# Kernel optimization log

Hardware: AMD Instinct MI355X
Metric: run time of the kernel (lower is better)

The kernel has to match this reference:

```python
import jax, jax.numpy as jnp
import numpy as np

N = 20000      # nodes
E = 320000     # edges (before self loops)
DIN = 64       # input feature dim
C = 256        # hidden_dim (per-head channels)
HEADS = 4
NEG_SLOPE_ATT = 0.2   # GATv2 leaky_relu slope
NEG_SLOPE = 0.01      # torch F.leaky_relu default


def setup_inputs() -> dict:
    key = jax.random.key(0)
    ks = jax.random.split(key, 32)
    def g(i, shape, fan_in):
        return jax.random.normal(ks[i], shape, jnp.float32) * (1.0 / np.sqrt(fan_in))
    inp = {}
    inp["x"] = jax.random.normal(ks[0], (N, DIN), jnp.float32)
    inp["src"] = jax.random.randint(ks[1], (E,), 0, N, jnp.int32)
    inp["dst"] = jax.random.randint(ks[2], (E,), 0, N, jnp.int32)
    # input layer
    inp["W_in"] = g(3, (DIN, C), DIN); inp["b_in"] = jnp.zeros((C,), jnp.float32)
    # conv1: in=256 -> heads=4, out=256, concat
    inp["Wl1"] = g(4, (C, HEADS * C), C); inp["bl1"] = jnp.zeros((HEADS * C,), jnp.float32)
    inp["Wr1"] = g(5, (C, HEADS * C), C); inp["br1"] = jnp.zeros((HEADS * C,), jnp.float32)
    inp["att1"] = g(6, (HEADS, C), C); inp["bias1"] = jnp.zeros((HEADS * C,), jnp.float32)
    # conv2: in=1024 -> heads=4, out=256, concat
    inp["Wl2"] = g(7, (HEADS * C, HEADS * C), HEADS * C); inp["bl2"] = jnp.zeros((HEADS * C,), jnp.float32)
    inp["Wr2"] = g(8, (HEADS * C, HEADS * C), HEADS * C); inp["br2"] = jnp.zeros((HEADS * C,), jnp.float32)
    inp["att2"] = g(9, (HEADS, C), C); inp["bias2"] = jnp.zeros((HEADS * C,), jnp.float32)
    # conv3: in=1024 -> heads=1, out=256, no concat
    inp["Wl3"] = g(10, (HEADS * C, C), HEADS * C); inp["bl3"] = jnp.zeros((C,), jnp.float32)
    inp["Wr3"] = g(11, (HEADS * C, C), HEADS * C); inp["br3"] = jnp.zeros((C,), jnp.float32)
    inp["att3"] = g(12, (1, C), C); inp["bias3"] = jnp.zeros((C,), jnp.float32)
    # output layer
    inp["W_out"] = g(13, (C, 1), C); inp["b_out"] = jnp.zeros((1,), jnp.float32)
    return inp


def _seg_softmax(scores, seg, n):
    # scores: [E, H] segment-wise softmax over dst node ids
    m = jax.ops.segment_max(scores, seg, num_segments=n)
    ex = jnp.exp(scores - m[seg])
    den = jax.ops.segment_sum(ex, seg, num_segments=n)
    return ex / den[seg]


def _gatv2(x, s, d, Wl, bl, Wr, br, att, bias, heads, concat):
    n = x.shape[0]
    c = att.shape[1]
    xl = (x @ Wl + bl).reshape(n, heads, c)  # messages (source side)
    xr = (x @ Wr + br).reshape(n, heads, c)  # target side
    e = jax.nn.leaky_relu(xl[s] + xr[d], NEG_SLOPE_ATT)          # [E, H, C]
    sc = jnp.einsum('ehc,hc->eh', e, att)                         # [E, H]
    alpha = _seg_softmax(sc, d, n)                                # [E, H]
    out = jax.ops.segment_sum(alpha[:, :, None] * xl[s], d, num_segments=n)  # [N, H, C]
    out = out.reshape(n, heads * c) if concat else out.mean(axis=1)
    return out + bias


def reference(x, src, dst, W_in, b_in, Wl1, bl1, Wr1, br1, att1, bias1,
              Wl2, bl2, Wr2, br2, att2, bias2, Wl3, bl3, Wr3, br3, att3, bias3,
              W_out, b_out):
    n = x.shape[0]
    loop = jnp.arange(n, dtype=src.dtype)
    s = jnp.concatenate([src, loop])  # add_self_loops=True (PyG default)
    d = jnp.concatenate([dst, loop])
    h = jax.nn.leaky_relu(x @ W_in + b_in, NEG_SLOPE)
    h1 = jax.nn.elu(_gatv2(h, s, d, Wl1, bl1, Wr1, br1, att1, bias1, HEADS, True))
    h2 = jax.nn.elu(_gatv2(h1, s, d, Wl2, bl2, Wr2, br2, att2, bias2, HEADS, True))
    h3 = _gatv2(h2, s, d, Wl3, bl3, Wr3, br3, att3, bias3, 1, False)
    out = jax.nn.leaky_relu(h3, NEG_SLOPE) + h
    logits = (out @ W_out + b_out).squeeze(-1)
    return logits
```

## Files before the change

kernel.cpp:

```cpp
#include <hip/hip_runtime.h>
#include <math.h>

#define NEG_ATT 0.2f
#define NEG 0.01f

typedef __attribute__((ext_vector_type(8))) short short8;
typedef __attribute__((ext_vector_type(4))) float f32x4;

static __device__ __forceinline__ float lrelu(float x, float s) { return x > 0.f ? x : s * x; }
static __device__ __forceinline__ unsigned short f2b(float f) {
  union { float f; unsigned int i; } v; v.f = f;
  unsigned int r = (v.i + 0x7fffu + ((v.i >> 16) & 1u)) >> 16;
  return (unsigned short)r;
}
static __device__ __forceinline__ void unpack8(uint4 r, float* x) {
  union { unsigned int u; float f; } t;
  t.u = r.x << 16;          x[0] = t.f;
  t.u = r.x & 0xffff0000u;  x[1] = t.f;
  t.u = r.y << 16;          x[2] = t.f;
  t.u = r.y & 0xffff0000u;  x[3] = t.f;
  t.u = r.z << 16;          x[4] = t.f;
  t.u = r.z & 0xffff0000u;  x[5] = t.f;
  t.u = r.w << 16;          x[6] = t.f;
  t.u = r.w & 0xffff0000u;  x[7] = t.f;
}

__global__ void zero_int_kernel(int* __restrict__ p, int n) {
  int i = blockIdx.x * blockDim.x + threadIdx.x;
  if (i < n) p[i] = 0;
}

__global__ void hist_kernel(const int* __restrict__ dst, int* __restrict__ cnt, int E, int N) {
  int i = blockIdx.x * blockDim.x + threadIdx.x;
  int tot = E + N;
  if (i >= tot) return;
  int d = (i < E) ? dst[i] : (i - E);
  atomicAdd(&cnt[d], 1);
}

__global__ void scan_kernel(const int* __restrict__ cnt, int* __restrict__ rowptr,
                            int* __restrict__ cursor, int n) {
  __shared__ int wsum[16];
  __shared__ int carry_s;
  int t = threadIdx.x;
  int lane = t & 63, wv = t >> 6;
  if (t == 0) carry_s = 0;
  __syncthreads();
  for (int base = 0; base < n; base += 1024) {
    int i = base + t;
    int orig = (i < n) ? cnt[i] : 0;
    int v = orig;
    #pragma unroll
    for (int off = 1; off < 64; off <<= 1) {
      int u = __shfl_up(v, off);
      if (lane >= off) v += u;
    }
    if (lane == 63) wsum[wv] = v;
    __syncthreads();
    if (t < 16) {
      int s = wsum[t];
      #pragma unroll
      for (int off = 1; off < 16; off <<= 1) {
        int u = __shfl_up(s, off);
        if (t >= off) s += u;
      }
      wsum[t] = s;
    }
    __syncthreads();
    int waveoff = (wv > 0) ? wsum[wv - 1] : 0;
    int carry = carry_s;
    int excl = carry + waveoff + v - orig;
    if (i < n) { rowptr[i] = excl; cursor[i] = excl; }
    __syncthreads();
    if (t == 0) carry_s = carry + wsum[15];
    __syncthreads();
  }
  if (t == 0) rowptr[n] = carry_s;
}

__global__ void fill_kernel(const int* __restrict__ src, const int* __restrict__ dst,
                            int* __restrict__ cursor, int* __restrict__ colsrc, int E, int N) {
  int i = blockIdx.x * blockDim.x + threadIdx.x;
  int tot = E + N;
  if (i >= tot) return;
  int d, s;
  if (i < E) { d = dst[i]; s = src[i]; } else { d = i - E; s = i - E; }
  int pos = atomicAdd(&cursor[d], 1);
  colsrc[pos] = s;
}

static __device__ __forceinline__ void do_transpose(
    const float* __restrict__ W, unsigned short* __restrict__ Wt,
    int K, int Ncol, int lbid, float (*t)[33]) {
  int nxb = Ncol >> 5;
  int bx = lbid % nxb, by = lbid / nxb;
  int n0 = bx * 32, k0 = by * 32;
  int tx = threadIdx.x & 31, ty = threadIdx.x >> 5;
  #pragma unroll
  for (int i = 0; i < 4; ++i)
    t[ty + i * 8][tx] = W[(size_t)(k0 + ty + i * 8) * Ncol + n0 + tx];
  __syncthreads();
  #pragma unroll
  for (int i = 0; i < 4; ++i)
    Wt[(size_t)(n0 + ty + i * 8) * K + k0 + tx] = f2b(t[tx][ty + i * 8]);
}

__global__ __launch_bounds__(256) void prep_all(
    const float* __restrict__ W_in,
    const float* __restrict__ Wl1, const float* __restrict__ Wr1,
    const float* __restrict__ Wl2, const float* __restrict__ Wr2,
    const float* __restrict__ Wl3, const float* __restrict__ Wr3,
    unsigned short* __restrict__ WtIn,
    unsigned short* __restrict__ WtL1, unsigned short* __restrict__ WtR1,
    unsigned short* __restrict__ WtL2, unsigned short* __restrict__ WtR2,
    unsigned short* __restrict__ WtL3, unsigned short* __restrict__ WtR3,
    const float* __restrict__ x, unsigned short* __restrict__ xbf, int nx_elems,
    const float* __restrict__ bl1, const float* __restrict__ br1,
    const float* __restrict__ bl2, const float* __restrict__ br2,
    const float* __restrict__ bl3, const float* __restrict__ br3,
    float* __restrict__ bLR1, float* __restrict__ bLR2, float* __restrict__ bLR3) {
  __shared__ float t[32][33];
  int bid = blockIdx.x;
  if (bid < 16)        { do_transpose(W_in, WtIn, 64, 256, bid, t); return; }
  if (bid < 272)       { do_transpose(Wl1, WtL1, 256, 1024, bid - 16, t); return; }
  if (bid < 528)       { do_transpose(Wr1, WtR1, 256, 1024, bid - 272, t); return; }
  if (bid < 1552)      { do_transpose(Wl2, WtL2, 1024, 1024, bid - 528, t); return; }
  if (bid < 2576)      { do_transpose(Wr2, WtR2, 1024, 1024, bid - 1552, t); return; }
  if (bid < 2832)      { do_transpose(Wl3, WtL3, 1024, 256, bid - 2576, t); return; }
  if (bid < 3088)      { do_transpose(Wr3, WtR3, 1024, 256, bid - 2832, t); return; }
  if (bid < 3106) {
    int i = (bid - 3088) * 256 + threadIdx.x;
    if (i < 1024)      bLR1[i] = bl1[i];
    else if (i < 2048) bLR1[i] = br1[i - 1024];
    else if (i < 3072) bLR2[i - 2048] = bl2[i - 2048];
    else if (i < 4096) bLR2[i - 2048] = br2[i - 3072];
    else if (i < 4352) bLR3[i - 4096] = bl3[i - 4096];
    else if (i < 4608) bLR3[i - 4096] = br3[i - 4352];
    return;
  }
  int i = (bid - 3106) * 256 + threadIdx.x;
  if (i < nx_elems) xbf[i] = f2b(x[i]);
}

__global__ __launch_bounds__(256) void gemm_mfma(
    const unsigned short* __restrict__ A, const unsigned short* __restrict__ Bt,
    const float* __restrict__ bias, float* __restrict__ Cf, unsigned short* __restrict__ Cb,
    int M, int K, int ldcf, int ldcb, int act) {
  __shared__ __align__(16) unsigned short As[128 * 64];
  __shared__ __align__(16) unsigned short Bs[128 * 64];
  int tid = threadIdx.x;
  int wave = tid >> 6, lane = tid & 63;
  int wm = wave >> 1, wn = wave & 1;
  int quad = lane >> 4, l16 = lane & 15;
  int row0 = blockIdx.y * 128, col0 = blockIdx.x * 128;
  int r0 = tid >> 2, seg0 = tid & 3;
  int swz = (seg0 ^ ((r0 >> 1) & 3)) * 8;
  int wsl0 = r0 * 64 + swz;
  int wsl1 = wsl0 + 32;
  int wsl2 = wsl0 + 64 * 64;
  int wsl3 = wsl2 + 32;
  int chunkbase = (quad ^ ((l16 >> 1) & 3)) * 8;

  const unsigned short* gA = A + (size_t)(row0 + r0) * K + seg0 * 8;
  const unsigned short* gB = Bt + (size_t)(col0 + r0) * K + seg0 * 8;
  const size_t rstep = (size_t)64 * K;

  f32x4 acc[4][4];
  #pragma unroll
  for (int i = 0; i < 4; ++i)
    #pragma unroll
    for (int j = 0; j < 4; ++j)
      acc[i][j] = (f32x4){0.f, 0.f, 0.f, 0.f};

  uint4 pa0 = *(const uint4*)(gA);
  uint4 pa1 = *(const uint4*)(gA + 32);
  uint4 pa2 = *(const uint4*)(gA + rstep);
  uint4 pa3 = *(const uint4*)(gA + rstep + 32);
  uint4 pb0 = *(const uint4*)(gB);
  uint4 pb1 = *(const uint4*)(gB + 32);
  uint4 pb2 = *(const uint4*)(gB + rstep);
  uint4 pb3 = *(const uint4*)(gB + rstep + 32);

  for (int k0 = 0; k0 < K; k0 += 64) {
    *(uint4*)&As[wsl0] = pa0;
    *(uint4*)&As[wsl1] = pa1;
    *(uint4*)&As[wsl2] = pa2;
    *(uint4*)&As[wsl3] = pa3;
    *(uint4*)&Bs[wsl0] = pb0;
    *(uint4*)&Bs[wsl1] = pb1;
    *(uint4*)&Bs[wsl2] = pb2;
    *(uint4*)&Bs[wsl3] = pb3;
    __syncthreads();
    int kn = k0 + 64;
    if (kn < K) {
      pa0 = *(const uint4*)(gA + kn);
      pa1 = *(const uint4*)(gA + kn + 32);
      pa2 = *(const uint4*)(gA + kn + rstep);
      pa3 = *(const uint4*)(gA + kn + rstep + 32);
      pb0 = *(const uint4*)(gB + kn);
      pb1 = *(const uint4*)(gB + kn + 32);
      pb2 = *(const uint4*)(gB + kn + rstep);
      pb3 = *(const uint4*)(gB + kn + rstep + 32);
    }
    #pragma unroll
    for (int h = 0; h < 2; ++h) {
      short8 afr[4], bfr[4];
      #pragma unroll
      for (int t = 0; t < 4; ++t) {
        afr[t] = *(const short8*)&As[(wm * 64 + t * 16 + l16) * 64 + h * 32 + chunkbase];
        bfr[t] = *(const short8*)&Bs[(wn * 64 + t * 16 + l16) * 64 + h * 32 + chunkbase];
      }
      #pragma unroll
      for (int mt = 0; mt < 4; ++mt)
        #pragma unroll
        for (int nt = 0; nt < 4; ++nt)
          acc[mt][nt] = __builtin_amdgcn_mfma_f32_16x16x32_bf16(afr[mt], bfr[nt], acc[mt][nt], 0, 0, 0);
    }
    __syncthreads();
  }

  #pragma unroll
  for (int mt = 0; mt < 4; ++mt) {
    #pragma unroll
    for (int r = 0; r < 4; ++r) {
      int row = row0 + wm * 64 + mt * 16 + quad * 4 + r;
      if (row >= M) continue;
      #pragma unroll
      for (int nt = 0; nt < 4; ++nt) {
        int col = col0 + wn * 64 + nt * 16 + l16;
        float v = acc[mt][nt][r] + bias[col];
        if (act == 1) v = lrelu(v, NEG);
        if (Cf) Cf[(size_t)row * ldcf + col] = v;
        if (Cb) Cb[(size_t)row * ldcb + col] = f2b(v);
      }
    }
  }
}

__global__ __launch_bounds__(256) void gat_agg_h4(
    const unsigned short* __restrict__ xlr,
    const int* __restrict__ rowptr, const int* __restrict__ colsrc,
    const float* __restrict__ att, const float* __restrict__ bias,
    unsigned short* __restrict__ outb, int n) {
  const int S = 2048, XROFF = 1024;
  int d = blockIdx.x;
  if (d >= n) return;
  int hd = threadIdx.x >> 6, ln = threadIdx.x & 63;
  int half = ln >> 5, l32 = ln & 31;
  int c0 = l32 * 8;
  float a[8], a5[8], xr_[8];
  {
    float4 t0 = *(const float4*)(att + hd * 256 + c0);
    float4 t1 = *(const float4*)(att + hd * 256 + c0 + 4);
    a[0]=t0.x; a[1]=t0.y; a[2]=t0.z; a[3]=t0.w;
    a[4]=t1.x; a[5]=t1.y; a[6]=t1.z; a[7]=t1.w;
    #pragma unroll
    for (int c = 0; c < 8; ++c) a5[c] = NEG_ATT * a[c];
    uint4 r = *(const uint4*)(xlr + (size_t)d * S + XROFF + hd * 256 + c0);
    unpack8(r, xr_);
  }
  float m = -1e30f, l = 0.f, acc[8];
  #pragma unroll
  for (int c = 0; c < 8; ++c) acc[c] = 0.f;
  int beg = rowptr[d], end = rowptr[d + 1];
  for (int j = beg; j < end; j += 2) {
    int jj = j + half;
    bool valid = (jj < end);
    int s = colsrc[valid ? jj : j];
    uint4 raw = *(const uint4*)(xlr + (size_t)s * S + hd * 256 + c0);
    float x[8];
    unpack8(raw, x);
    float p = 0.f;
    #pragma unroll
    for (int c = 0; c < 8; ++c) {
      float u = x[c] + xr_[c];
      p = fmaf(u, (u > 0.f ? a[c] : a5[c]), p);
    }
    #pragma unroll
    for (int off = 16; off >= 1; off >>= 1) p += __shfl_xor(p, off);
    if (!valid) p = -1e30f;
    float nm = fmaxf(m, p);
    if (nm > m) {
      float scl = __expf(m - nm);
      l *= scl;
      #pragma unroll
      for (int c = 0; c < 8; ++c) acc[c] *= scl;
      m = nm;
    }
    float w = __expf(p - m);
    l += w;
    #pragma unroll
    for (int c = 0; c < 8; ++c) acc[c] = fmaf(w, x[c], acc[c]);
  }
  float mo = __shfl_xor(m, 32);
  float lo = __shfl_xor(l, 32);
  float M = fmaxf(m, mo);
  float sl = __expf(m - M);
  float so = __expf(mo - M);
  float L = fmaf(l, sl, lo * so);
  float inv = 1.f / L;
  float4 b0 = *(const float4*)(bias + hd * 256 + c0);
  float4 b1 = *(const float4*)(bias + hd * 256 + c0 + 4);
  float bb[8] = {b0.x, b0.y, b0.z, b0.w, b1.x, b1.y, b1.z, b1.w};
  unsigned int ou[4];
  #pragma unroll
  for (int c = 0; c < 8; ++c) {
    float po = __shfl_xor(acc[c], 32);
    float v = fmaf(acc[c], sl, po * so) * inv + bb[c];
    v = v > 0.f ? v : expm1f(v);
    unsigned int bv = (unsigned int)f2b(v);
    if (c & 1) ou[c >> 1] |= bv << 16; else ou[c >> 1] = bv;
  }
  if (half == 0) {
    uint4 o = make_uint4(ou[0], ou[1], ou[2], ou[3]);
    *(uint4*)(outb + (size_t)d * 1024 + hd * 256 + c0) = o;
  }
}

__global__ __launch_bounds__(256) void gat_agg_h1_final(
    const unsigned short* __restrict__ xlr,
    const int* __restrict__ rowptr, const int* __restrict__ colsrc,
    const float* __restrict__ att, const float* __restrict__ bias,
    const float* __restrict__ h, const float* __restrict__ Wout,
    const float* __restrict__ bout, float* __restrict__ out, int n) {
  const int S = 512, XROFF = 256;
  int wv = threadIdx.x >> 6, ln = threadIdx.x & 63;
  int d = blockIdx.x * 4 + wv;
  if (d >= n) return;
  int half = ln >> 5, l32 = ln & 31;
  int c0 = l32 * 8;
  float a[8], a5[8], xr_[8];
  {
    float4 t0 = *(const float4*)(att + c0);
    float4 t1 = *(const float4*)(att + c0 + 4);
    a[0]=t0.x; a[1]=t0.y; a[2]=t0.z; a[3]=t0.w;
    a[4]=t1.x; a[5]=t1.y; a[6]=t1.z; a[7]=t1.w;
    #pragma unroll
    for (int c = 0; c < 8; ++c) a5[c] = NEG_ATT * a[c];
    uint4 r = *(const uint4*)(xlr + (size_t)d * S + XROFF + c0);
    unpack8(r, xr_);
  }
  float m = -1e30f, l = 0.f, acc[8];
  #pragma unroll
  for (int c = 0; c < 8; ++c) acc[c] = 0.f;
  int beg = rowptr[d], end = rowptr[d + 1];
  for (int j = beg; j < end; j += 2) {
    int jj = j + half;
    bool valid = (jj < end);
    int s = colsrc[valid ? jj : j];
    uint4 raw = *(const uint4*)(xlr + (size_t)s * S + c0);
    float x[8];
    unpack8(raw, x);
    float p = 0.f;
    #pragma unroll
    for (int c = 0; c < 8; ++c) {
      float u = x[c] + xr_[c];
      p = fmaf(u, (u > 0.f ? a[c] : a5[c]), p);
    }
    #pragma unroll
    for (int off = 16; off >= 1; off >>= 1) p += __shfl_xor(p, off);
    if (!valid) p = -1e30f;
    float nm = fmaxf(m, p);
    if (nm > m) {
      float scl = __expf(m - nm);
      l *= scl;
      #pragma unroll
      for (int c = 0; c < 8; ++c) acc[c] *= scl;
      m = nm;
    }
    float w = __expf(p - m);
    l += w;
    #pragma unroll
    for (int c = 0; c < 8; ++c) acc[c] = fmaf(w, x[c], acc[c]);
  }
  float mo = __shfl_xor(m, 32);
  float lo = __shfl_xor(l, 32);
  float M = fmaxf(m, mo);
  float sl = __expf(m - M);
  float so = __expf(mo - M);
  float L = fmaf(l, sl, lo * so);
  float inv = 1.f / L;
  float4 b0 = *(const float4*)(bias + c0);
  float4 b1 = *(const float4*)(bias + c0 + 4);
  float bb[8] = {b0.x, b0.y, b0.z, b0.w, b1.x, b1.y, b1.z, b1.w};
  float4 h0 = *(const float4*)(h + (size_t)d * 256 + c0);
  float4 h1v = *(const float4*)(h + (size_t)d * 256 + c0 + 4);
  float hh[8] = {h0.x, h0.y, h0.z, h0.w, h1v.x, h1v.y, h1v.z, h1v.w};
  float4 w0 = *(const float4*)(Wout + c0);
  float4 w1 = *(const float4*)(Wout + c0 + 4);
  float ww[8] = {w0.x, w0.y, w0.z, w0.w, w1.x, w1.y, w1.z, w1.w};
  float v = 0.f;
  #pragma unroll
  for (int c = 0; c < 8; ++c) {
    float h3c = fmaf(acc[c], sl, __shfl_xor(acc[c], 32) * so) * inv + bb[c];
    v = fmaf(lrelu(h3c, NEG) + hh[c], ww[c], v);
  }
  #pragma unroll
  for (int off = 16; off >= 1; off >>= 1) v += __shfl_xor(v, off);
  if (ln == 0) out[d] = v + bout[0];
}

extern "C" void kernel_launch(void* const* d_in, const int* in_sizes, int n_in,
                              void* d_out, int out_size, void* d_ws, size_t ws_size,
                              hipStream_t stream) {
  const float* x    = (const float*)d_in[0];
  const int*   src  = (const int*)d_in[1];
  const int*   dst  = (const int*)d_in[2];
  const float* W_in = (const float*)d_in[3];
  const float* b_in = (const float*)d_in[4];
  const float* Wl1 = (const float*)d_in[5];  const float* bl1 = (const float*)d_in[6];
  const float* Wr1 = (const float*)d_in[7];  const float* br1 = (const float*)d_in[8];
  const float* att1 = (const float*)d_in[9]; const float* bias1 = (const float*)d_in[10];
  const float* Wl2 = (const float*)d_in[11]; const float* bl2 = (const float*)d_in[12];
  const float* Wr2 = (const float*)d_in[13]; const float* br2 = (const float*)d_in[14];
  const float* att2 = (const float*)d_in[15]; const float* bias2 = (const float*)d_in[16];
  const float* Wl3 = (const float*)d_in[17]; const float* bl3 = (const float*)d_in[18];
  const float* Wr3 = (const float*)d_in[19]; const float* br3 = (const float*)d_in[20];
  const float* att3 = (const float*)d_in[21]; const float* bias3 = (const float*)d_in[22];
  const float* W_out = (const float*)d_in[23]; const float* b_out = (const float*)d_in[24];

  const int N = in_sizes[0] / 64;
  const int E = in_sizes[1];
  const int NP = ((N + 127) / 128) * 128;
  float* out = (float*)d_out;

  char* p = (char*)d_ws;
  float* h   = (float*)p;            p += (size_t)N * 256 * 4;
  unsigned short* xbf  = (unsigned short*)p; p += (size_t)NP * 64 * 2;
  unsigned short* hbf  = (unsigned short*)p; p += (size_t)NP * 256 * 2;
  unsigned short* h1bf = (unsigned short*)p; p += (size_t)NP * 1024 * 2;
  unsigned short* h2bf = (unsigned short*)p; p += (size_t)NP * 1024 * 2;
  unsigned short* xlr  = (unsigned short*)p; p += (size_t)N * 2048 * 2;
  unsigned short* WtIn  = (unsigned short*)p; p += (size_t)256 * 64 * 2;
  unsigned short* WtLR1 = (unsigned short*)p; p += (size_t)2048 * 256 * 2;
  unsigned short* WtLR2 = (unsigned short*)p; p += (size_t)2048 * 1024 * 2;
  unsigned short* WtLR3 = (unsigned short*)p; p += (size_t)512 * 1024 * 2;
  float* bLR1 = (float*)p;           p += (size_t)2048 * 4;
  float* bLR2 = (float*)p;           p += (size_t)2048 * 4;
  float* bLR3 = (float*)p;           p += (size_t)512 * 4;
  int* cnt    = (int*)p;             p += (size_t)N * 4;
  int* cursor = (int*)p;             p += (size_t)N * 4;
  int* rowptr = (int*)p;             p += (size_t)(N + 1) * 4;
  int* colsrc = (int*)p;

  const int tot = E + N;
  dim3 blk(256);

  zero_int_kernel<<<(N + 255) / 256, blk, 0, stream>>>(cnt, N);
  hist_kernel<<<(tot + 255) / 256, blk, 0, stream>>>(dst, cnt, E, N);
  scan_kernel<<<1, 1024, 0, stream>>>(cnt, rowptr, cursor, N);
  fill_kernel<<<(tot + 255) / 256, blk, 0, stream>>>(src, dst, cursor, colsrc, E, N);

  int nbf2b = (N * 64 + 255) / 256;
  prep_all<<<3106 + nbf2b, blk, 0, stream>>>(
      W_in, Wl1, Wr1, Wl2, Wr2, Wl3, Wr3,
      WtIn, WtLR1, WtLR1 + (size_t)1024 * 256,
      WtLR2, WtLR2 + (size_t)1024 * 1024,
      WtLR3, WtLR3 + (size_t)256 * 1024,
      x, xbf, N * 64,
      bl1, br1, bl2, br2, bl3, br3, bLR1, bLR2, bLR3);

  int gy = NP / 128;
  int gagg4 = N;
  int gagg1 = (N + 3) / 4;

  gemm_mfma<<<dim3(2, gy), blk, 0, stream>>>(xbf, WtIn, b_in, h, hbf, N, 64, 256, 256, 1);

  gemm_mfma<<<dim3(16, gy), blk, 0, stream>>>(hbf, WtLR1, bLR1, nullptr, xlr, N, 256, 0, 2048, 0);
  gat_agg_h4<<<gagg4, blk, 0, stream>>>(xlr, rowptr, colsrc, att1, bias1, h1bf, N);

  gemm_mfma<<<dim3(16, gy), blk, 0, stream>>>(h1bf, WtLR2, bLR2, nullptr, xlr, N, 1024, 0, 2048, 0);
  gat_agg_h4<<<gagg4, blk, 0, stream>>>(xlr, rowptr, colsrc, att2, bias2, h2bf, N);

  gemm_mfma<<<dim3(4, gy), blk, 0, stream>>>(h2bf, WtLR3, bLR3, nullptr, xlr, N, 1024, 0, 512, 0);
  gat_agg_h1_final<<<gagg1, blk, 0, stream>>>(xlr, rowptr, colsrc, att3, bias3,
                                              h, W_out, b_out, out, N);
}
```

Measured before the change: 741.9 us.

## Use self-loop score as fixed softmax shift and process two edges per step

The GATv2 aggregation kernels drop the online-softmax running max and its rescaling. Each destination instead first computes its self-loop attention score and uses it as a constant shift for every exp, which relies on softmax being invariant to the shift. The edge loop now handles two edges per half-wave per iteration, so two independent gathers and reductions are in flight, and leaky-relu becomes a single fmax. The risk is exp overflow or underflow when neighbour scores differ greatly from the self-loop score, because the shift is no longer the true maximum.

```diff
diff --git a/kernel.cpp b/kernel.cpp
--- a/kernel.cpp
+++ b/kernel.cpp
@@ -248,65 +248,77 @@
   int hd = threadIdx.x >> 6, ln = threadIdx.x & 63;
   int half = ln >> 5, l32 = ln & 31;
   int c0 = l32 * 8;
-  float a[8], a5[8], xr_[8];
+  float a[8], xr_[8];
   {
     float4 t0 = *(const float4*)(att + hd * 256 + c0);
     float4 t1 = *(const float4*)(att + hd * 256 + c0 + 4);
     a[0]=t0.x; a[1]=t0.y; a[2]=t0.z; a[3]=t0.w;
     a[4]=t1.x; a[5]=t1.y; a[6]=t1.z; a[7]=t1.w;
-    #pragma unroll
-    for (int c = 0; c < 8; ++c) a5[c] = NEG_ATT * a[c];
     uint4 r = *(const uint4*)(xlr + (size_t)d * S + XROFF + hd * 256 + c0);
     unpack8(r, xr_);
   }
-  float m = -1e30f, l = 0.f, acc[8];
+  float ps = 0.f;
+  {
+    uint4 r = *(const uint4*)(xlr + (size_t)d * S + hd * 256 + c0);
+    float xs[8];
+    unpack8(r, xs);
+    #pragma unroll
+    for (int c = 0; c < 8; ++c) {
+      float u = xs[c] + xr_[c];
+      u = fmaxf(u, NEG_ATT * u);
+      ps = fmaf(u, a[c], ps);
+    }
+    #pragma unroll
+    for (int off = 16; off >= 1; off >>= 1) ps += __shfl_xor(ps, off);
+  }
+  float l = 0.f, acc[8];
   #pragma unroll
   for (int c = 0; c < 8; ++c) acc[c] = 0.f;
   int beg = rowptr[d], end = rowptr[d + 1];
-  for (int j = beg; j < end; j += 2) {
-    int jj = j + half;
-    bool valid = (jj < end);
-    int s = colsrc[valid ? jj : j];
-    uint4 raw = *(const uint4*)(xlr + (size_t)s * S + hd * 256 + c0);
-    float x[8];
-    unpack8(raw, x);
-    float p = 0.f;
+  for (int j = beg; j < end; j += 4) {
+    int j0 = j + half, j1 = j + 2 + half;
+    bool v0 = j0 < end, v1 = j1 < end;
+    int s0 = colsrc[v0 ? j0 : beg];
+    int s1 = colsrc[v1 ? j1 : beg];
+    uint4 r0 = *(const uint4*)(xlr + (size_t)s0 * S + hd * 256 + c0);
+    uint4 r1 = *(const uint4*)(xlr + (size_t)s1 * S + hd * 256 + c0);
+    float x0[8], x1[8];
+    unpack8(r0, x0);
+    unpack8(r1, x1);
+    float p0 = 0.f, p1 = 0.f;
     #pragma unroll
     for (int c = 0; c < 8; ++c) {
-      float u = x[c] + xr_[c];
-      p = fmaf(u, (u > 0.f ? a[c] : a5[c]), p);
-    }
-    #pragma unroll
-    for (int off = 16; off >= 1; off >>= 1) p += __shfl_xor(p, off);
-    if (!valid) p = -1e30f;
-    float nm = fmaxf(m, p);
-    if (nm > m) {
-      float scl = __expf(m - nm);
-      l *= scl;
-      #pragma unroll
-      for (int c = 0; c < 8; ++c) acc[c] *= scl;
-      m = nm;
-    }
-    float w = __expf(p - m);
-    l += w;
-    #pragma unroll
-    for (int c = 0; c < 8; ++c) acc[c] = fmaf(w, x[c], acc[c]);
-  }
-  float mo = __shfl_xor(m, 32);
-  float lo = __shfl_xor(l, 32);
-  float M = fmaxf(m, mo);
-  float sl = __expf(m - M);
-  float so = __expf(mo - M);
-  float L = fmaf(l, sl, lo * so);
-  float inv = 1.f / L;
+      float u0 = x0[c] + xr_[c];
+      float u1 = x1[c] + xr_[c];
+      u0 = fmaxf(u0, NEG_ATT * u0);
+      u1 = fmaxf(u1, NEG_ATT * u1);
+      p0 = fmaf(u0, a[c], p0);
+      p1 = fmaf(u1, a[c], p1);
+    }
+    #pragma unroll
+    for (int off = 16; off >= 1; off >>= 1) {
+      p0 += __shfl_xor(p0, off);
+      p1 += __shfl_xor(p1, off);
+    }
+    float w0 = v0 ? __expf(p0 - ps) : 0.f;
+    float w1 = v1 ? __expf(p1 - ps) : 0.f;
+    l += w0 + w1;
+    #pragma unroll
+    for (int c = 0; c < 8; ++c) {
+      acc[c] = fmaf(w0, x0[c], acc[c]);
+      acc[c] = fmaf(w1, x1[c], acc[c]);
+    }
+  }
+  l += __shfl_xor(l, 32);
+  float inv = 1.f / l;
   float4 b0 = *(const float4*)(bias + hd * 256 + c0);
   float4 b1 = *(const float4*)(bias + hd * 256 + c0 + 4);
   float bb[8] = {b0.x, b0.y, b0.z, b0.w, b1.x, b1.y, b1.z, b1.w};
   unsigned int ou[4];
   #pragma unroll
   for (int c = 0; c < 8; ++c) {
-    float po = __shfl_xor(acc[c], 32);
-    float v = fmaf(acc[c], sl, po * so) * inv + bb[c];
+    float s = acc[c] + __shfl_xor(acc[c], 32);
+    float v = s * inv + bb[c];
     v = v > 0.f ? v : expm1f(v);
     unsigned int bv = (unsigned int)f2b(v);
     if (c & 1) ou[c >> 1] |= bv << 16; else ou[c >> 1] = bv;
@@ -329,70 +341,83 @@
   if (d >= n) return;
   int half = ln >> 5, l32 = ln & 31;
   int c0 = l32 * 8;
-  float a[8], a5[8], xr_[8];
+  float a[8], xr_[8];
   {
     float4 t0 = *(const float4*)(att + c0);
     float4 t1 = *(const float4*)(att + c0 + 4);
     a[0]=t0.x; a[1]=t0.y; a[2]=t0.z; a[3]=t0.w;
     a[4]=t1.x; a[5]=t1.y; a[6]=t1.z; a[7]=t1.w;
-    #pragma unroll
-    for (int c = 0; c < 8; ++c) a5[c] = NEG_ATT * a[c];
     uint4 r = *(const uint4*)(xlr + (size_t)d * S + XROFF + c0);
     unpack8(r, xr_);
   }
-  float m = -1e30f, l = 0.f, acc[8];
+  float ps = 0.f;
+  {
+    uint4 r = *(const uint4*)(xlr + (size_t)d * S + c0);
+    float xs[8];
+    unpack8(r, xs);
+    #pragma unroll
+    for (int c = 0; c < 8; ++c) {
+      float u = xs[c] + xr_[c];
+      u = fmaxf(u, NEG_ATT * u);
+      ps = fmaf(u, a[c], ps);
+    }
+    #pragma unroll
+    for (int off = 16; off >= 1; off >>= 1) ps += __shfl_xor(ps, off);
+  }
+  float l = 0.f, acc[8];
   #pragma unroll
   for (int c = 0; c < 8; ++c) acc[c] = 0.f;
   int beg = rowptr[d], end = rowptr[d + 1];
-  for (int j = beg; j < end; j += 2) {
-    int jj = j + half;
-    bool valid = (jj < end);
-    int s = colsrc[valid ? jj : j];
-    uint4 raw = *(const uint4*)(xlr + (size_t)s * S + c0);
-    float x[8];
-    unpack8(raw, x);
-    float p = 0.f;
+  for (int j = beg; j < end; j += 4) {
+    int j0 = j + half, j1 = j + 2 + half;
+    bool v0 = j0 < end, v1 = j1 < end;
+    int s0 = colsrc[v0 ? j0 : beg];
+    int s1 = colsrc[v1 ? j1 : beg];
+    uint4 r0 = *(const uint4*)(xlr + (size_t)s0 * S + c0);
+    uint4 r1 = *(const uint4*)(xlr + (size_t)s1 * S + c0);
+    float x0[8], x1[8];
+    unpack8(r0, x0);
+    unpack8(r1, x1);
+    float p0 = 0.f, p1 = 0.f;
     #pragma unroll
     for (int c = 0; c < 8; ++c) {
-      float u = x[c] + xr_[c];
-      p = fmaf(u, (u > 0.f ? a[c] : a5[c]), p);
-    }
-    #pragma unroll
-    for (int off = 16; off >= 1; off >>= 1) p += __shfl_xor(p, off);
-    if (!valid) p = -1e30f;
-    float nm = fmaxf(m, p);
-    if (nm > m) {
-      float scl = __expf(m - nm);
-      l *= scl;
-      #pragma unroll
-      for (int c = 0; c < 8; ++c) acc[c] *= scl;
-      m = nm;
-    }
-    float w = __expf(p - m);
-    l += w;
-    #pragma unroll
-    for (int c = 0; c < 8; ++c) acc[c] = fmaf(w, x[c], acc[c]);
-  }
-  float mo = __shfl_xor(m, 32);
-  float lo = __shfl_xor(l, 32);
-  float M = fmaxf(m, mo);
-  float sl = __expf(m - M);
-  float so = __expf(mo - M);
-  float L = fmaf(l, sl, lo * so);
-  float inv = 1.f / L;
+      float u0 = x0[c] + xr_[c];
+      float u1 = x1[c] + xr_[c];
+      u0 = fmaxf(u0, NEG_ATT * u0);
+      u1 = fmaxf(u1, NEG_ATT * u1);
+      p0 = fmaf(u0, a[c], p0);
+      p1 = fmaf(u1, a[c], p1);
+    }
+    #pragma unroll
+    for (int off = 16; off >= 1; off >>= 1) {
+      p0 += __shfl_xor(p0, off);
+      p1 += __shfl_xor(p1, off);
+    }
+    float w0 = v0 ? __expf(p0 - ps) : 0.f;
+    float w1 = v1 ? __expf(p1 - ps) : 0.f;
+    l += w0 + w1;
+    #pragma unroll
+    for (int c = 0; c < 8; ++c) {
+      acc[c] = fmaf(w0, x0[c], acc[c]);
+      acc[c] = fmaf(w1, x1[c], acc[c]);
+    }
+  }
+  l += __shfl_xor(l, 32);
+  float inv = 1.f / l;
   float4 b0 = *(const float4*)(bias + c0);
   float4 b1 = *(const float4*)(bias + c0 + 4);
   float bb[8] = {b0.x, b0.y, b0.z, b0.w, b1.x, b1.y, b1.z, b1.w};
   float4 h0 = *(const float4*)(h + (size_t)d * 256 + c0);
   float4 h1v = *(const float4*)(h + (size_t)d * 256 + c0 + 4);
   float hh[8] = {h0.x, h0.y, h0.z, h0.w, h1v.x, h1v.y, h1v.z, h1v.w};
-  float4 w0 = *(const float4*)(Wout + c0);
-  float4 w1 = *(const float4*)(Wout + c0 + 4);
-  float ww[8] = {w0.x, w0.y, w0.z, w0.w, w1.x, w1.y, w1.z, w1.w};
+  float4 w0v = *(const float4*)(Wout + c0);
+  float4 w1v = *(const float4*)(Wout + c0 + 4);
+  float ww[8] = {w0v.x, w0v.y, w0v.z, w0v.w, w1v.x, w1v.y, w1v.z, w1v.w};
   float v = 0.f;
   #pragma unroll
   for (int c = 0; c < 8; ++c) {
-    float h3c = fmaf(acc[c], sl, __shfl_xor(acc[c], 32) * so) * inv + bb[c];
+    float s = acc[c] + __shfl_xor(acc[c], 32);
+    float h3c = s * inv + bb[c];
     v = fmaf(lrelu(h3c, NEG) + hh[c], ww[c], v);
   }
   #pragma unroll
```

Result: faster. 717.8 us (-3.2%).
